# Performance work log

Measured on AMD Instinct MI355X. Metric: run time of the kernel, lower is better.

## Reference

```python
import jax, jax.numpy as jnp
import numpy as np

N = 100000      # nodes
E = 600000      # directed edges
D_IN = 128
D_H = 128
D_OUT = 128
EPS = 1e-5      # BatchNorm eps


def setup_inputs() -> dict:
    key = jax.random.key(0)
    ks = jax.random.split(key, 6)
    x = jax.random.normal(ks[0], (N, D_IN), dtype=jnp.float32)
    edge_index = jax.random.randint(ks[1], (2, E), 0, N, dtype=jnp.int64)
    s1 = 1.0 / np.sqrt(D_IN)
    s2 = 1.0 / np.sqrt(D_H)
    W1 = jax.random.uniform(ks[2], (D_IN, D_H), minval=-s1, maxval=s1, dtype=jnp.float32)
    b1 = jnp.zeros((D_H,), jnp.float32)
    gamma1 = jnp.ones((D_H,), jnp.float32)
    beta1 = jnp.zeros((D_H,), jnp.float32)
    W2 = jax.random.uniform(ks[3], (D_H, D_OUT), minval=-s2, maxval=s2, dtype=jnp.float32)
    b2 = jnp.zeros((D_OUT,), jnp.float32)
    return dict(x=x, edge_index=edge_index, W1=W1, b1=b1,
                gamma1=gamma1, beta1=beta1, W2=W2, b2=b2)


def _gcn_conv(x, W, b, src, dst):
    # PyG GCNConv: h = D^{-1/2} (A + I) D^{-1/2} (x @ W) + b
    n = x.shape[0]
    h = x @ W                                   # [N, d_out]
    loop = jnp.arange(n, dtype=src.dtype)
    s = jnp.concatenate([src, loop])            # self loops appended
    d = jnp.concatenate([dst, loop])
    deg = jax.ops.segment_sum(jnp.ones_like(d, jnp.float32), d, num_segments=n)
    dinv = jax.lax.rsqrt(deg)                   # deg >= 1 after self loops
    norm = dinv[s] * dinv[d]                    # [E + N]
    agg = jax.ops.segment_sum(h[s] * norm[:, None], d, num_segments=n)  # [N, d_out]
    return agg + b


def reference(x, edge_index, W1, b1, gamma1, beta1, W2, b2):
    src, dst = edge_index[0], edge_index[1]
    # layer 0: GCNConv -> BatchNorm1d (training batch stats) -> ReLU (dropout p=0)
    h = _gcn_conv(x, W1, b1, src, dst)
    mean = h.mean(axis=0)
    var = h.var(axis=0)                         # biased variance, as torch BN
    h = (h - mean) * jax.lax.rsqrt(var + EPS) * gamma1 + beta1
    h = jax.nn.relu(h)
    # final layer: GCNConv only
    return _gcn_conv(h, W2, b2, src, dst)
```

## Files before the change

### kernel.cpp

```cpp
#include <hip/hip_runtime.h>

#define D 128
#define EPSV 1e-5f

typedef __attribute__((ext_vector_type(8))) short bf16x8;
typedef __attribute__((ext_vector_type(4))) float f32x4;

__device__ __forceinline__ short f2bf(float f){
  unsigned u = __float_as_uint(f);
  u += 0x7fffu + ((u >> 16) & 1u);
  return (short)(u >> 16);
}
__device__ __forceinline__ float bflo(unsigned u){ return __uint_as_float(u << 16); }
__device__ __forceinline__ float bfhi(unsigned u){ return __uint_as_float(u & 0xffff0000u); }
__device__ __forceinline__ float bf2f(short s){ return __uint_as_float(((unsigned)(unsigned short)s) << 16); }
__device__ __forceinline__ unsigned packbf(float a, float b){
  unsigned lo = (unsigned short)f2bf(a);
  unsigned hi = (unsigned short)f2bf(b);
  return lo | (hi << 16);
}

__global__ void k_init(int N, int E, const int* __restrict__ ei, int* __restrict__ flag,
                       int* __restrict__ deg, int* __restrict__ fill, float* __restrict__ gpart,
                       int* __restrict__ sflg,
                       const float* __restrict__ W1, const float* __restrict__ W2,
                       short* __restrict__ w1t, short* __restrict__ w2t){
  int i = blockIdx.x*blockDim.x + threadIdx.x;
  if (i < N){ deg[i] = 0; fill[i] = 0; }
  if (i < D*D){
    int j = i >> 7, k = i & 127;
    w1t[i] = f2bf(W1[k*D + j]);
    w2t[i] = f2bf(W2[k*D + j]);
  }
  if (i < 2048) gpart[i] = 0.f;
  if (i < 128) sflg[i] = 0;
  if (blockIdx.x == 0){
    __shared__ int any;
    int t = threadIdx.x;
    if (t == 0) any = 0;
    __syncthreads();
    if (2*t+1 < 2*E && ei[2*t+1] != 0) atomicOr(&any, 1);
    __syncthreads();
    if (t == 0) flag[0] = (any == 0) ? 1 : 0;
  }
}

__global__ void k_scan(const int* __restrict__ deg, int N, int* __restrict__ rowp,
                       float* __restrict__ dinv, int* __restrict__ s_agg,
                       int* __restrict__ s_inc, int* __restrict__ s_flg){
  __shared__ int sh[256];
  __shared__ int s_ex;
  int b = blockIdx.x, t = threadIdx.x;
  int base = b*1024 + t*4;
  int c0 = (base+0 < N) ? deg[base+0] : 0;
  int c1 = (base+1 < N) ? deg[base+1] : 0;
  int c2 = (base+2 < N) ? deg[base+2] : 0;
  int c3 = (base+3 < N) ? deg[base+3] : 0;
  int s = c0 + c1 + c2 + c3;
  sh[t] = s; __syncthreads();
  for (int d = 1; d < 256; d <<= 1){
    int v = (t >= d) ? sh[t-d] : 0;
    __syncthreads();
    sh[t] += v;
    __syncthreads();
  }
  int total = sh[255];
  if (t == 0){
    atomicExch(&s_agg[b], total);
    __threadfence();
    atomicExch(&s_flg[b], 1);
    int ex = 0;
    for (int i = b-1; i >= 0; ){
      int f;
      while ((f = atomicAdd(&s_flg[i], 0)) == 0) __builtin_amdgcn_s_sleep(1);
      if (f == 2){ ex += atomicAdd(&s_inc[i], 0); break; }
      ex += atomicAdd(&s_agg[i], 0); --i;
    }
    atomicExch(&s_inc[b], ex + total);
    __threadfence();
    atomicExch(&s_flg[b], 2);
    s_ex = ex;
  }
  __syncthreads();
  int o = sh[t] - s + s_ex;
  if (base+0 < N){ rowp[base+0] = o; dinv[base+0] = rsqrtf((float)(c0+1)); } o += c0;
  if (base+1 < N){ rowp[base+1] = o; dinv[base+1] = rsqrtf((float)(c1+1)); } o += c1;
  if (base+2 < N){ rowp[base+2] = o; dinv[base+2] = rsqrtf((float)(c2+1)); } o += c2;
  if (base+3 < N){ rowp[base+3] = o; dinv[base+3] = rsqrtf((float)(c3+1)); }
}

__global__ void k_scatter(const int* __restrict__ ei, int E, const int* __restrict__ flag,
                          const int* __restrict__ rowp, int* __restrict__ fill,
                          const float* __restrict__ dinv, int2* __restrict__ epack){
  int e = blockIdx.x*blockDim.x + threadIdx.x;
  if (e >= E) return;
  int s, d;
  if (flag[0]){ s = ei[2*e]; d = ei[2*E + 2*e]; }
  else        { s = ei[e];   d = ei[E + e];     }
  int pos = rowp[d] + atomicAdd(&fill[d], 1);
  int2 ev; ev.x = s; ev.y = __float_as_int(dinv[s] * dinv[d]);
  epack[pos] = ev;
}

template<int MODE>
__global__ __launch_bounds__(256, 2) void k_gemm(const void* __restrict__ A,
                                const short* __restrict__ BT, short* __restrict__ C, int N,
                                const float* __restrict__ gpart, const float* __restrict__ gamma,
                                const float* __restrict__ beta,
                                const int* __restrict__ ei, int E, const int* __restrict__ flag,
                                int* __restrict__ deg, int ngemmb){
  if (MODE == 1 && (int)blockIdx.x >= ngemmb){
    int cb = blockIdx.x - ngemmb;
    int e0 = cb*1024 + threadIdx.x;
    int f = flag[0];
    #pragma unroll
    for (int r = 0; r < 4; ++r){
      int e = e0 + r*256;
      if (e < E){
        int d = f ? ei[2*E + 2*e] : ei[E + e];
        atomicAdd(&deg[d], 1);
      }
    }
    return;
  }
  __shared__ short ldsB[16384];
  __shared__ short ldsC[4*2048];
  __shared__ __align__(16) float s_sc[128];
  __shared__ __align__(16) float s_sh[128];
  int w = threadIdx.x >> 6;
  int lane = threadIdx.x & 63;
  int m = lane & 15, quad = lane >> 4;

  if (MODE == 2 && threadIdx.x < 128){
    int f = threadIdx.x;
    float s = 0.f, q = 0.f;
    #pragma unroll
    for (int i = 0; i < 8; ++i){ s += gpart[i*256 + f]; q += gpart[i*256 + 128 + f]; }
    float inv = 1.f / (float)N;
    float mean = s * inv;
    float var  = q * inv - mean*mean;
    float sc = gamma[f] * rsqrtf(var + EPSV);
    s_sc[f] = sc;
    s_sh[f] = beta[f] - mean * sc;
  }
  {
    const bf16x8* BTv = (const bf16x8*)BT;
    bf16x8* Bw = (bf16x8*)ldsB;
    for (int g = threadIdx.x; g < 2048; g += 256){
      int row = g >> 4, ch = g & 15;
      Bw[row*16 + (ch ^ (row & 15))] = BTv[g];
    }
  }
  __syncthreads();
  const bf16x8* Bv = (const bf16x8*)ldsB;
  short* cw = ldsC + w*2048;

  int tiles = (N + 31) >> 5;
  int wid = blockIdx.x*4 + w;
  int wstride = ngemmb*4;
  for (int tile = wid; tile < tiles; tile += wstride){
    int r0 = tile << 5;
    bf16x8 a[2][4];
    #pragma unroll
    for (int g = 0; g < 2; ++g){
      int row = r0 + g*16 + m;
      if (row >= N) row = N - 1;
      #pragma unroll
      for (int kc = 0; kc < 4; ++kc){
        int k0 = kc*32 + quad*8;
        if (MODE == 1){
          const float* Af = (const float*)A + (size_t)row*D + k0;
          float4 u = *(const float4*)Af;
          float4 v = *(const float4*)(Af + 4);
          bf16x8 tv;
          tv[0]=f2bf(u.x); tv[1]=f2bf(u.y); tv[2]=f2bf(u.z); tv[3]=f2bf(u.w);
          tv[4]=f2bf(v.x); tv[5]=f2bf(v.y); tv[6]=f2bf(v.z); tv[7]=f2bf(v.w);
          a[g][kc] = tv;
        } else {
          bf16x8 raw = *(const bf16x8*)((const short*)A + (size_t)row*D + k0);
          float4 s0v = *(const float4*)(s_sc + k0);
          float4 s1v = *(const float4*)(s_sc + k0 + 4);
          float4 h0v = *(const float4*)(s_sh + k0);
          float4 h1v = *(const float4*)(s_sh + k0 + 4);
          bf16x8 tv;
          tv[0] = f2bf(fmaxf(fmaf(bf2f(raw[0]), s0v.x, h0v.x), 0.f));
          tv[1] = f2bf(fmaxf(fmaf(bf2f(raw[1]), s0v.y, h0v.y), 0.f));
          tv[2] = f2bf(fmaxf(fmaf(bf2f(raw[2]), s0v.z, h0v.z), 0.f));
          tv[3] = f2bf(fmaxf(fmaf(bf2f(raw[3]), s0v.w, h0v.w), 0.f));
          tv[4] = f2bf(fmaxf(fmaf(bf2f(raw[4]), s1v.x, h1v.x), 0.f));
          tv[5] = f2bf(fmaxf(fmaf(bf2f(raw[5]), s1v.y, h1v.y), 0.f));
          tv[6] = f2bf(fmaxf(fmaf(bf2f(raw[6]), s1v.z, h1v.z), 0.f));
          tv[7] = f2bf(fmaxf(fmaf(bf2f(raw[7]), s1v.w, h1v.w), 0.f));
          a[g][kc] = tv;
        }
      }
    }
    f32x4 acc[2][8];
    #pragma unroll
    for (int g = 0; g < 2; ++g)
      #pragma unroll
      for (int c = 0; c < 8; ++c) acc[g][c] = (f32x4){0.f,0.f,0.f,0.f};
    #pragma unroll
    for (int kc = 0; kc < 4; ++kc){
      bf16x8 bb[8];
      #pragma unroll
      for (int c = 0; c < 8; ++c)
        bb[c] = Bv[(c*16 + m)*16 + ((kc*4 + quad) ^ m)];
      #pragma unroll
      for (int g = 0; g < 2; ++g)
        #pragma unroll
        for (int c = 0; c < 8; ++c)
          acc[g][c] = __builtin_amdgcn_mfma_f32_16x16x32_bf16(bb[c], a[g][kc], acc[g][c], 0, 0, 0);
    }
    #pragma unroll
    for (int g = 0; g < 2; ++g){
      #pragma unroll
      for (int c = 0; c < 8; ++c){
        uint2 v;
        v.x = packbf(acc[g][c][0], acc[g][c][1]);
        v.y = packbf(acc[g][c][2], acc[g][c][3]);
        int x = c*2 + (quad >> 1);
        *(uint2*)&cw[m*128 + ((x ^ m) << 3) + ((quad & 1) << 2)] = v;
      }
      asm volatile("s_waitcnt lgkmcnt(0)" ::: "memory");
      #pragma unroll
      for (int rg = 0; rg < 4; ++rg){
        int lrow = rg*4 + quad;
        int rr = r0 + g*16 + lrow;
        uint4 v = *(const uint4*)&cw[lrow*128 + ((m ^ lrow) << 3)];
        if (rr < N) *(uint4*)(C + (size_t)rr*D + m*8) = v;
      }
      asm volatile("s_waitcnt lgkmcnt(0)" ::: "memory");
    }
  }
}

template<int OUTF32>
__global__ __launch_bounds__(256) void k_agg(const short* __restrict__ H, const int* __restrict__ rowp,
        const int* __restrict__ deg, const int2* __restrict__ epack, const float* __restrict__ dinv,
        const float* __restrict__ bias, void* __restrict__ out, int N, float* __restrict__ gpart){
  int w = threadIdx.x >> 6, p = threadIdx.x & 63;
  int wid = blockIdx.x*4 + w, wstride = gridDim.x*4;
  const unsigned* Hu = (const unsigned*)H;
  float S0=0.f, S1=0.f, Q0=0.f, Q1=0.f;
  float bb0=0.f, bb1=0.f;
  if (OUTF32){ bb0 = bias[2*p]; bb1 = bias[2*p+1]; }

  int n = wid;
  int start=0, cnt=0; float d1=0.f; unsigned u=0; int2 ev; ev.x=0; ev.y=0;
  if (n < N){
    start = rowp[n]; cnt = deg[n]; d1 = dinv[n];
    u = Hu[(size_t)n*64 + p];
    int nb = cnt < 64 ? cnt : 64;
    if (p < nb) ev = epack[start + p];
  }
  while (n < N){
    int n2 = n + wstride;
    int start2=0, cnt2=0; float d12=0.f; unsigned u2=0; int2 ev2; ev2.x=0; ev2.y=0;
    if (n2 < N){
      start2 = rowp[n2]; cnt2 = deg[n2]; d12 = dinv[n2];
      u2 = Hu[(size_t)n2*64 + p];
      int nb2 = cnt2 < 64 ? cnt2 : 64;
      if (p < nb2) ev2 = epack[start2 + p];
    }
    float w0 = d1*d1;
    float a0 = w0 * bflo(u), a1 = w0 * bfhi(u);
    int nb = cnt < 64 ? cnt : 64;
    for (int j = 0; j < nb; j += 8){
      int s0 = __shfl(ev.x, j+0), s1 = __shfl(ev.x, j+1);
      int s2 = __shfl(ev.x, j+2), s3 = __shfl(ev.x, j+3);
      int s4 = __shfl(ev.x, j+4), s5 = __shfl(ev.x, j+5);
      int s6 = __shfl(ev.x, j+6), s7 = __shfl(ev.x, j+7);
      float f0 = __int_as_float(__shfl(ev.y, j+0));
      float f1 = __int_as_float(__shfl(ev.y, j+1));
      float f2 = __int_as_float(__shfl(ev.y, j+2));
      float f3 = __int_as_float(__shfl(ev.y, j+3));
      float f4 = __int_as_float(__shfl(ev.y, j+4));
      float f5 = __int_as_float(__shfl(ev.y, j+5));
      float f6 = __int_as_float(__shfl(ev.y, j+6));
      float f7 = __int_as_float(__shfl(ev.y, j+7));
      unsigned u0 = Hu[(size_t)s0*64 + p], u1 = Hu[(size_t)s1*64 + p];
      unsigned u2g = Hu[(size_t)s2*64 + p], u3 = Hu[(size_t)s3*64 + p];
      unsigned u4 = Hu[(size_t)s4*64 + p], u5 = Hu[(size_t)s5*64 + p];
      unsigned u6 = Hu[(size_t)s6*64 + p], u7 = Hu[(size_t)s7*64 + p];
      a0 = fmaf(f0, bflo(u0), a0); a1 = fmaf(f0, bfhi(u0), a1);
      a0 = fmaf(f1, bflo(u1), a0); a1 = fmaf(f1, bfhi(u1), a1);
      a0 = fmaf(f2, bflo(u2g), a0); a1 = fmaf(f2, bfhi(u2g), a1);
      a0 = fmaf(f3, bflo(u3), a0); a1 = fmaf(f3, bfhi(u3), a1);
      a0 = fmaf(f4, bflo(u4), a0); a1 = fmaf(f4, bfhi(u4), a1);
      a0 = fmaf(f5, bflo(u5), a0); a1 = fmaf(f5, bfhi(u5), a1);
      a0 = fmaf(f6, bflo(u6), a0); a1 = fmaf(f6, bfhi(u6), a1);
      a0 = fmaf(f7, bflo(u7), a0); a1 = fmaf(f7, bfhi(u7), a1);
    }
    for (int base = 64; base < cnt; base += 64){
      int nbx = cnt - base; if (nbx > 64) nbx = 64;
      int2 evx; evx.x = 0; evx.y = 0;
      if (p < nbx) evx = epack[start + base + p];
      for (int j = 0; j < nbx; j += 8){
        #pragma unroll
        for (int q2 = 0; q2 < 8; ++q2){
          int sx = __shfl(evx.x, j+q2);
          float fx = __int_as_float(__shfl(evx.y, j+q2));
          unsigned ux = Hu[(size_t)sx*64 + p];
          a0 = fmaf(fx, bflo(ux), a0); a1 = fmaf(fx, bfhi(ux), a1);
        }
      }
    }
    if (OUTF32){
      float2 r; r.x = a0 + bb0; r.y = a1 + bb1;
      ((float2*)out)[(size_t)n*64 + p] = r;
    } else {
      ((unsigned*)out)[(size_t)n*64 + p] = packbf(a0, a1);
      S0 += a0; Q0 += a0*a0; S1 += a1; Q1 += a1*a1;
    }
    n = n2; start = start2; cnt = cnt2; d1 = d12; u = u2; ev = ev2;
  }
  if (!OUTF32){
    __shared__ float ls[1024];
    int base = w*256;
    ls[base + 2*p]       = S0;
    ls[base + 2*p + 1]   = S1;
    ls[base + 128 + 2*p]     = Q0;
    ls[base + 128 + 2*p + 1] = Q1;
    __syncthreads();
    int t = threadIdx.x;
    float v = ls[t] + ls[256 + t] + ls[512 + t] + ls[768 + t];
    atomicAdd(&gpart[(blockIdx.x & 7)*256 + t], v);
  }
}

extern "C" void kernel_launch(void* const* d_in, const int* in_sizes, int n_in,
                              void* d_out, int out_size, void* d_ws, size_t ws_size,
                              hipStream_t stream){
  const float* x   = (const float*)d_in[0];
  const int*   ei  = (const int*)  d_in[1];
  const float* W1  = (const float*)d_in[2];
  const float* g1  = (const float*)d_in[4];
  const float* be1 = (const float*)d_in[5];
  const float* W2  = (const float*)d_in[6];
  const float* b2  = (const float*)d_in[7];
  float* out = (float*)d_out;
  int N = in_sizes[0] / D;
  int E = in_sizes[1] / 2;

  char* w = (char*)d_ws;
  auto carve = [&](size_t bytes)->char*{ char* p = w; w += (bytes + 255) & ~(size_t)255; return p; };
  int*   flag  = (int*)  carve(256);
  int*   degA  = (int*)  carve((size_t)N*4);
  int*   fillA = (int*)  carve((size_t)N*4);
  float* dinvA = (float*)carve((size_t)N*4);
  int*   rowp  = (int*)  carve((size_t)N*4);
  int*   sagg  = (int*)  carve(512);
  int*   sinc  = (int*)  carve(512);
  int*   sflg  = (int*)  carve(512);
  int2*  epack = (int2*) carve((size_t)E*8);
  float* gpart = (float*)carve(2048*4);
  short* w1t   = (short*)carve((size_t)D*D*2);
  short* w2t   = (short*)carve((size_t)D*D*2);
  short* h1    = (short*)carve((size_t)N*D*2);
  short* hb    = (short*)carve((size_t)N*D*2);

  const int TB = 256;
  int EB  = (E + TB - 1) / TB;
  int NBt = (N + TB - 1) / TB;
  int NB1024 = (N + 1023) / 1024;
  int GEMMB = 512;
  int CNTB  = (E + 1023) / 1024;
  int AGGB  = 2048;

  k_init    <<<NBt, TB, 0, stream>>>(N, E, ei, flag, degA, fillA, gpart, sflg, W1, W2, w1t, w2t);
  k_gemm<1> <<<GEMMB + CNTB, 256, 0, stream>>>(x, w1t, h1, N, nullptr, nullptr, nullptr,
                                               ei, E, flag, degA, GEMMB);
  k_scan    <<<NB1024, 256, 0, stream>>>(degA, N, rowp, dinvA, sagg, sinc, sflg);
  k_scatter <<<EB, TB, 0, stream>>>(ei, E, flag, rowp, fillA, dinvA, epack);
  k_agg<0>  <<<AGGB, 256, 0, stream>>>(h1, rowp, degA, epack, dinvA, nullptr, hb, N, gpart);
  k_gemm<2> <<<GEMMB, 256, 0, stream>>>(hb, w2t, h1, N, gpart, g1, be1,
                                        nullptr, 0, nullptr, nullptr, GEMMB);
  k_agg<1>  <<<AGGB, 256, 0, stream>>>(h1, rowp, degA, epack, dinvA, b2, out, N, nullptr);
}
```

Measured before the change: 259.2 us.

## Process two nodes per wavefront in aggregation with 8-byte gathers

```diff
diff --git a/kernel.cpp b/kernel.cpp
--- a/kernel.cpp
+++ b/kernel.cpp
@@ -103,7 +103,7 @@
 }
 
 template<int MODE>
-__global__ __launch_bounds__(256, 2) void k_gemm(const void* __restrict__ A,
+__global__ __launch_bounds__(256, 3) void k_gemm(const void* __restrict__ A,
                                 const short* __restrict__ BT, short* __restrict__ C, int N,
                                 const float* __restrict__ gpart, const float* __restrict__ gamma,
                                 const float* __restrict__ beta,
@@ -240,92 +240,84 @@
         const int* __restrict__ deg, const int2* __restrict__ epack, const float* __restrict__ dinv,
         const float* __restrict__ bias, void* __restrict__ out, int N, float* __restrict__ gpart){
   int w = threadIdx.x >> 6, p = threadIdx.x & 63;
+  int q = p & 31, hb32 = p & 32;
   int wid = blockIdx.x*4 + w, wstride = gridDim.x*4;
-  const unsigned* Hu = (const unsigned*)H;
-  float S0=0.f, S1=0.f, Q0=0.f, Q1=0.f;
-  float bb0=0.f, bb1=0.f;
-  if (OUTF32){ bb0 = bias[2*p]; bb1 = bias[2*p+1]; }
-
-  int n = wid;
-  int start=0, cnt=0; float d1=0.f; unsigned u=0; int2 ev; ev.x=0; ev.y=0;
-  if (n < N){
-    start = rowp[n]; cnt = deg[n]; d1 = dinv[n];
-    u = Hu[(size_t)n*64 + p];
-    int nb = cnt < 64 ? cnt : 64;
-    if (p < nb) ev = epack[start + p];
-  }
-  while (n < N){
-    int n2 = n + wstride;
-    int start2=0, cnt2=0; float d12=0.f; unsigned u2=0; int2 ev2; ev2.x=0; ev2.y=0;
-    if (n2 < N){
-      start2 = rowp[n2]; cnt2 = deg[n2]; d12 = dinv[n2];
-      u2 = Hu[(size_t)n2*64 + p];
-      int nb2 = cnt2 < 64 ? cnt2 : 64;
-      if (p < nb2) ev2 = epack[start2 + p];
-    }
+  const uint2* Hu2 = (const uint2*)H;
+  float S0=0.f,S1=0.f,S2=0.f,S3=0.f,Q0=0.f,Q1=0.f,Q2=0.f,Q3=0.f;
+  float4 b4 = {0.f,0.f,0.f,0.f};
+  if (OUTF32) b4 = *(const float4*)(bias + 4*q);
+  int pairs = (N + 1) >> 1;
+  for (int pr = wid; pr < pairs; pr += wstride){
+    int n = 2*pr + (p >> 5);
+    bool valid = n < N;
+    int start = 0, cnt = 0; float d1 = 0.f;
+    if (valid){ start = rowp[n]; cnt = deg[n]; d1 = dinv[n]; }
+    uint2 self; self.x = 0; self.y = 0;
+    if (valid) self = Hu2[(size_t)n*32 + q];
+    int2 ev; ev.x = 0; ev.y = 0;
+    if (q < (cnt < 32 ? cnt : 32)) ev = epack[start + q];
+    int co = __shfl(cnt, p ^ 32);
+    int maxcF = cnt > co ? cnt : co;
+    int maxc = maxcF < 32 ? maxcF : 32;
     float w0 = d1*d1;
-    float a0 = w0 * bflo(u), a1 = w0 * bfhi(u);
-    int nb = cnt < 64 ? cnt : 64;
-    for (int j = 0; j < nb; j += 8){
-      int s0 = __shfl(ev.x, j+0), s1 = __shfl(ev.x, j+1);
-      int s2 = __shfl(ev.x, j+2), s3 = __shfl(ev.x, j+3);
-      int s4 = __shfl(ev.x, j+4), s5 = __shfl(ev.x, j+5);
-      int s6 = __shfl(ev.x, j+6), s7 = __shfl(ev.x, j+7);
-      float f0 = __int_as_float(__shfl(ev.y, j+0));
-      float f1 = __int_as_float(__shfl(ev.y, j+1));
-      float f2 = __int_as_float(__shfl(ev.y, j+2));
-      float f3 = __int_as_float(__shfl(ev.y, j+3));
-      float f4 = __int_as_float(__shfl(ev.y, j+4));
-      float f5 = __int_as_float(__shfl(ev.y, j+5));
-      float f6 = __int_as_float(__shfl(ev.y, j+6));
-      float f7 = __int_as_float(__shfl(ev.y, j+7));
-      unsigned u0 = Hu[(size_t)s0*64 + p], u1 = Hu[(size_t)s1*64 + p];
-      unsigned u2g = Hu[(size_t)s2*64 + p], u3 = Hu[(size_t)s3*64 + p];
-      unsigned u4 = Hu[(size_t)s4*64 + p], u5 = Hu[(size_t)s5*64 + p];
-      unsigned u6 = Hu[(size_t)s6*64 + p], u7 = Hu[(size_t)s7*64 + p];
-      a0 = fmaf(f0, bflo(u0), a0); a1 = fmaf(f0, bfhi(u0), a1);
-      a0 = fmaf(f1, bflo(u1), a0); a1 = fmaf(f1, bfhi(u1), a1);
-      a0 = fmaf(f2, bflo(u2g), a0); a1 = fmaf(f2, bfhi(u2g), a1);
-      a0 = fmaf(f3, bflo(u3), a0); a1 = fmaf(f3, bfhi(u3), a1);
-      a0 = fmaf(f4, bflo(u4), a0); a1 = fmaf(f4, bfhi(u4), a1);
-      a0 = fmaf(f5, bflo(u5), a0); a1 = fmaf(f5, bfhi(u5), a1);
-      a0 = fmaf(f6, bflo(u6), a0); a1 = fmaf(f6, bfhi(u6), a1);
-      a0 = fmaf(f7, bflo(u7), a0); a1 = fmaf(f7, bfhi(u7), a1);
-    }
-    for (int base = 64; base < cnt; base += 64){
-      int nbx = cnt - base; if (nbx > 64) nbx = 64;
+    float a0 = w0*bflo(self.x), a1 = w0*bfhi(self.x);
+    float a2 = w0*bflo(self.y), a3 = w0*bfhi(self.y);
+    for (int j = 0; j < maxc; j += 8){
+      int ss[8]; float ff[8];
+      #pragma unroll
+      for (int t = 0; t < 8; ++t){
+        ss[t] = __shfl(ev.x, hb32 + j + t);
+        ff[t] = __int_as_float(__shfl(ev.y, hb32 + j + t));
+      }
+      uint2 uu[8];
+      #pragma unroll
+      for (int t = 0; t < 8; ++t) uu[t] = Hu2[(size_t)ss[t]*32 + q];
+      #pragma unroll
+      for (int t = 0; t < 8; ++t){
+        a0 = fmaf(ff[t], bflo(uu[t].x), a0); a1 = fmaf(ff[t], bfhi(uu[t].x), a1);
+        a2 = fmaf(ff[t], bflo(uu[t].y), a2); a3 = fmaf(ff[t], bfhi(uu[t].y), a3);
+      }
+    }
+    for (int base2 = 32; base2 < maxcF; base2 += 32){
       int2 evx; evx.x = 0; evx.y = 0;
-      if (p < nbx) evx = epack[start + base + p];
-      for (int j = 0; j < nbx; j += 8){
+      int rem = cnt - base2;
+      if (rem > 0 && q < (rem < 32 ? rem : 32)) evx = epack[start + base2 + q];
+      int mb = maxcF - base2; mb = mb < 32 ? mb : 32;
+      for (int j = 0; j < mb; j += 8){
         #pragma unroll
-        for (int q2 = 0; q2 < 8; ++q2){
-          int sx = __shfl(evx.x, j+q2);
-          float fx = __int_as_float(__shfl(evx.y, j+q2));
-          unsigned ux = Hu[(size_t)sx*64 + p];
-          a0 = fmaf(fx, bflo(ux), a0); a1 = fmaf(fx, bfhi(ux), a1);
+        for (int t = 0; t < 8; ++t){
+          int sx = __shfl(evx.x, hb32 + j + t);
+          float fx = __int_as_float(__shfl(evx.y, hb32 + j + t));
+          uint2 ux = Hu2[(size_t)sx*32 + q];
+          a0 = fmaf(fx, bflo(ux.x), a0); a1 = fmaf(fx, bfhi(ux.x), a1);
+          a2 = fmaf(fx, bflo(ux.y), a2); a3 = fmaf(fx, bfhi(ux.y), a3);
         }
       }
     }
     if (OUTF32){
-      float2 r; r.x = a0 + bb0; r.y = a1 + bb1;
-      ((float2*)out)[(size_t)n*64 + p] = r;
+      if (valid){
+        float4 r; r.x = a0 + b4.x; r.y = a1 + b4.y; r.z = a2 + b4.z; r.w = a3 + b4.w;
+        *(float4*)((float*)out + (size_t)n*D + 4*q) = r;
+      }
     } else {
-      ((unsigned*)out)[(size_t)n*64 + p] = packbf(a0, a1);
-      S0 += a0; Q0 += a0*a0; S1 += a1; Q1 += a1*a1;
-    }
-    n = n2; start = start2; cnt = cnt2; d1 = d12; u = u2; ev = ev2;
+      if (valid){
+        uint2 r; r.x = packbf(a0, a1); r.y = packbf(a2, a3);
+        ((uint2*)out)[(size_t)n*32 + q] = r;
+        S0 += a0; Q0 += a0*a0; S1 += a1; Q1 += a1*a1;
+        S2 += a2; Q2 += a2*a2; S3 += a3; Q3 += a3*a3;
+      }
+    }
   }
   if (!OUTF32){
-    __shared__ float ls[1024];
-    int base = w*256;
-    ls[base + 2*p]       = S0;
-    ls[base + 2*p + 1]   = S1;
-    ls[base + 128 + 2*p]     = Q0;
-    ls[base + 128 + 2*p + 1] = Q1;
-    __syncthreads();
-    int t = threadIdx.x;
-    float v = ls[t] + ls[256 + t] + ls[512 + t] + ls[768 + t];
-    atomicAdd(&gpart[(blockIdx.x & 7)*256 + t], v);
+    __shared__ float ls[256];
+    ls[threadIdx.x] = 0.f; __syncthreads();
+    int f = 4*q;
+    atomicAdd(&ls[f+0], S0); atomicAdd(&ls[f+1], S1);
+    atomicAdd(&ls[f+2], S2); atomicAdd(&ls[f+3], S3);
+    atomicAdd(&ls[128+f+0], Q0); atomicAdd(&ls[128+f+1], Q1);
+    atomicAdd(&ls[128+f+2], Q2); atomicAdd(&ls[128+f+3], Q3);
+    __syncthreads();
+    atomicAdd(&gpart[(blockIdx.x & 7)*256 + threadIdx.x], ls[threadIdx.x]);
   }
 }
 
@@ -364,7 +356,7 @@
   int EB  = (E + TB - 1) / TB;
   int NBt = (N + TB - 1) / TB;
   int NB1024 = (N + 1023) / 1024;
-  int GEMMB = 512;
+  int GEMMB = 768;
   int CNTB  = (E + 1023) / 1024;
   int AGGB  = 2048;
 
```

New measurement: 297.2 us. +14.6%, slower.
